# Kernel optimization log

Measured on AMD Instinct MI355X. Metric: run time of the kernel, lower is better.

The kernel has to match this reference:

```python
import jax, jax.numpy as jnp
import numpy as np

BETA = 0.25


def setup_inputs() -> dict:
    key = jax.random.key(0)
    k1, k2 = jax.random.split(key)
    B, D, H, W, K = 16, 256, 32, 32, 8192
    z_e = jax.random.normal(k1, (B, D, H, W), dtype=jnp.float32)
    # codebook init uniform(-1/K, 1/K) as in torch
    codebook = jax.random.uniform(k2, (K, D), dtype=jnp.float32,
                                  minval=-1.0 / K, maxval=1.0 / K)
    return {"z_e": z_e, "codebook": codebook}


def reference(z_e, codebook):
    B, D, H, W = z_e.shape
    K = codebook.shape[0]
    # (B, D, H, W) -> (BHW, D)
    z_flat = jnp.transpose(z_e, (0, 2, 3, 1)).reshape(-1, D)

    # distances computed under no_grad in torch -> stop_gradient here
    zf = jax.lax.stop_gradient(z_flat)
    cb = jax.lax.stop_gradient(codebook)
    # ||z||^2 + ||e||^2 - 2 z.e  -> (BHW, K)
    dist = ((zf * zf).sum(axis=1, keepdims=True)
            + (cb * cb).sum(axis=1)[None, :]
            - 2.0 * (zf @ cb.T))
    indices = jnp.argmin(dist, axis=1)  # (BHW,)

    # embedding gather, reshape back to (B, D, H, W)
    z_q_flat = codebook[indices]
    z_q = jnp.transpose(z_q_flat.reshape(B, H, W, D), (0, 3, 1, 2))

    # straight-through estimator
    z_q_st = z_e + jax.lax.stop_gradient(z_q - z_e)

    codebook_loss = jnp.mean((jax.lax.stop_gradient(z_q) - z_e) ** 2)
    commitment_loss = jnp.mean((z_q - jax.lax.stop_gradient(z_e)) ** 2)
    vq_loss = codebook_loss + BETA * commitment_loss

    # perplexity: one_hot(indices).mean(0) == counts / N
    N = z_flat.shape[0]
    counts = jnp.zeros((K,), dtype=z_flat.dtype).at[indices].add(1.0)
    avg_probs = counts / N
    perplexity = jnp.exp(-jnp.sum(avg_probs * jnp.log(avg_probs + 1e-10)))

    return (z_q_st, vq_loss, indices.reshape(B, H, W), perplexity)
```

## Files before the change

kernel.cpp:

```cpp
#include <hip/hip_runtime.h>

#define DD 256
#define KK 8192
#define HW 1024
#define NROWS 16384
#define NELEM 4194304
#define MT 32
#define MARGIN 6e-4f
#define WCAP 512
#define NT 256

typedef __attribute__((ext_vector_type(8))) short short8;
typedef __attribute__((ext_vector_type(4))) float f32x4;
typedef unsigned short ushort;
typedef unsigned int uint;
typedef unsigned long long u64;

__device__ __forceinline__ float np_pw128_sq(const float* p) {
  float r[8];
#pragma unroll
  for (int j = 0; j < 8; ++j) r[j] = __fmul_rn(p[j], p[j]);
  for (int i = 8; i < 128; i += 8) {
#pragma unroll
    for (int j = 0; j < 8; ++j)
      r[j] = __fadd_rn(r[j], __fmul_rn(p[i + j], p[i + j]));
  }
  return __fadd_rn(__fadd_rn(__fadd_rn(r[0], r[1]), __fadd_rn(r[2], r[3])),
                   __fadd_rn(__fadd_rn(r[4], r[5]), __fadd_rn(r[6], r[7])));
}

__device__ __forceinline__ ushort f2bf(float x) {
  uint u = __float_as_uint(x);
  u += 0x7FFF + ((u >> 16) & 1);
  return (ushort)(u >> 16);
}

__device__ __forceinline__ void emit8(ushort* __restrict__ zB, int g, int n16,
                                      int d0, const float* vv) {
  int s = d0 >> 5, q = (d0 >> 3) & 3;
  uint4 pk;
  pk.x = f2bf(vv[0]) | ((uint)f2bf(vv[1]) << 16);
  pk.y = f2bf(vv[2]) | ((uint)f2bf(vv[3]) << 16);
  pk.z = f2bf(vv[4]) | ((uint)f2bf(vv[5]) << 16);
  pk.w = f2bf(vv[6]) | ((uint)f2bf(vv[7]) << 16);
  *(uint4*)(zB + ((size_t)g * 512 + s * 64 + q * 16 + n16) * 8) = pk;
}

struct Top2 { float m1, m2; int i1; };

__device__ __forceinline__ void top2_upd(Top2& s, const f32x4 a,
                                         const f32x4 Bs, int ibase) {
  float d0 = fmaf(-2.f, a[0], Bs[0]);
  float d1 = fmaf(-2.f, a[1], Bs[1]);
  float d2 = fmaf(-2.f, a[2], Bs[2]);
  float d3 = fmaf(-2.f, a[3], Bs[3]);
  float lo01 = fminf(d0, d1), hi01 = fmaxf(d0, d1);
  int io01 = d1 < d0 ? ibase + 1 : ibase;
  float lo23 = fminf(d2, d3), hi23 = fmaxf(d2, d3);
  int io23 = d3 < d2 ? ibase + 3 : ibase + 2;
  float n1 = fminf(lo01, lo23);
  int ni = lo23 < lo01 ? io23 : io01;
  float n2 = fminf(fmaxf(lo01, lo23), fminf(hi01, hi23));
  s.m2 = fminf(fmaxf(s.m1, n1), fminf(s.m2, n2));
  s.i1 = n1 < s.m1 ? ni : s.i1;
  s.m1 = fminf(s.m1, n1);
}

__device__ __forceinline__ void top2_bfly(Top2& s, int off) {
  float om1 = __shfl_xor(s.m1, off);
  int oi1 = __shfl_xor(s.i1, off);
  float om2 = __shfl_xor(s.m2, off);
  s.m2 = fminf(fmaxf(s.m1, om1), fminf(s.m2, om2));
  s.i1 = om1 < s.m1 ? oi1 : s.i1;
  s.m1 = fminf(s.m1, om1);
}

__device__ __forceinline__ uint pack_m2(float m2, int i1) {
  uint u = __float_as_uint(m2);
  uint hi = u & 0xFFFF0000u;
  if ((u & 0x80000000u) && (u & 0xFFFFu)) hi += 0x10000u;
  return hi | (uint)i1;
}

__global__ __launch_bounds__(256) void vq_prep(const float* __restrict__ z,
                                               const float* __restrict__ cb,
                                               float* __restrict__ Bk,
                                               float* __restrict__ Arow,
                                               ushort* __restrict__ cbB,
                                               ushort* __restrict__ zB) {
  const int b = blockIdx.x, t = threadIdx.x;
  if (b < 32) {
    int k = b * 256 + t;
    const float* p = cb + (size_t)k * DD;
    Bk[k] = __fadd_rn(np_pw128_sq(p), np_pw128_sq(p + 128));
  } else if (b < 160) {
    int tid = (b - 32) * 256 + t;
    int n = tid >> 1, half = tid & 1;
    int bimg = n >> 10, hw = n & 1023;
    const float* zp = z + (size_t)bimg * DD * HW + hw;
    const int g = n >> 4, n16 = n & 15;
    const int dbase = half * 128;
    float r[8], vv[8];
#pragma unroll
    for (int j = 0; j < 8; ++j) {
      vv[j] = zp[(size_t)(dbase + j) * HW];
      r[j] = __fmul_rn(vv[j], vv[j]);
    }
    emit8(zB, g, n16, dbase, vv);
    for (int i = 8; i < 128; i += 8) {
      const int dd = dbase + i;
#pragma unroll
      for (int j = 0; j < 8; ++j) {
        vv[j] = zp[(size_t)(dd + j) * HW];
        r[j] = __fadd_rn(r[j], __fmul_rn(vv[j], vv[j]));
      }
      emit8(zB, g, n16, dd, vv);
    }
    float h = __fadd_rn(__fadd_rn(__fadd_rn(r[0], r[1]), __fadd_rn(r[2], r[3])),
                        __fadd_rn(__fadd_rn(r[4], r[5]), __fadd_rn(r[6], r[7])));
    float ho = __shfl_xor(h, 1);
    if (half == 0) Arow[n] = __fadd_rn(h, ho);
  } else {
    int tid = (b - 160) * 256 + t;
    int g = tid >> 9, s = (tid >> 6) & 7, lane = tid & 63;
    int code = g * 16 + (lane & 15);
    int dbase = s * 32 + (lane >> 4) * 8;
    const float* p = cb + (size_t)code * DD + dbase;
    ushort bb[8];
#pragma unroll
    for (int j = 0; j < 8; ++j) bb[j] = f2bf(p[j]);
    uint4 pk;
    pk.x = bb[0] | ((uint)bb[1] << 16);
    pk.y = bb[2] | ((uint)bb[3] << 16);
    pk.z = bb[4] | ((uint)bb[5] << 16);
    pk.w = bb[6] | ((uint)bb[7] << 16);
    *(uint4*)(cbB + (size_t)tid * 8) = pk;
  }
}

__global__ __launch_bounds__(256) void vq_screen(
    const ushort* __restrict__ zB, const ushort* __restrict__ cbB,
    const float* __restrict__ Bk, float* __restrict__ tA,
    uint* __restrict__ tB) {
  const int bid = blockIdx.x;
  const int rt = bid >> 1, cs = bid & 1;
  const int t = threadIdx.x;
  const int n0 = rt * MT;
  const int w = t >> 6, lane = t & 63;
  const int quad = lane >> 4, n16 = lane & 15;

  short8 aF[2][8];
#pragma unroll
  for (int rg = 0; rg < 2; ++rg) {
    const ushort* zp = zB + (size_t)(rt * 2 + rg) * 4096 + lane * 8;
#pragma unroll
    for (int s = 0; s < 8; ++s) aF[rg][s] = *(const short8*)(zp + s * 512);
  }

  const int gg0 = cs * 256 + w * 64;
  Top2 c0 = {3.4e38f, 3.4e38f, 0}, c1 = {3.4e38f, 3.4e38f, 0};

  short8 b0[8], b1[8];
  {
    const ushort* bp = cbB + (size_t)gg0 * 4096 + lane * 8;
#pragma unroll
    for (int s = 0; s < 8; ++s) b0[s] = *(const short8*)(bp + s * 512);
  }

  for (int gp = 0; gp < 32; ++gp) {
    const int gg = gg0 + gp * 2;
    {
      const ushort* bp = cbB + (size_t)(gg + 1) * 4096 + lane * 8;
#pragma unroll
      for (int s = 0; s < 8; ++s) b1[s] = *(const short8*)(bp + s * 512);
    }
    {
      f32x4 a0 = {0.f, 0.f, 0.f, 0.f}, a1 = {0.f, 0.f, 0.f, 0.f};
#pragma unroll
      for (int s = 0; s < 8; ++s) {
        a0 = __builtin_amdgcn_mfma_f32_16x16x32_bf16(b0[s], aF[0][s], a0, 0, 0, 0);
        a1 = __builtin_amdgcn_mfma_f32_16x16x32_bf16(b0[s], aF[1][s], a1, 0, 0, 0);
      }
      const f32x4 Bs = *(const f32x4*)(Bk + gg * 16 + quad * 4);
      top2_upd(c0, a0, Bs, quad * 4);
      top2_upd(c1, a1, Bs, quad * 4);
    }
    if (gp < 31) {
      const ushort* bp = cbB + (size_t)(gg + 2) * 4096 + lane * 8;
#pragma unroll
      for (int s = 0; s < 8; ++s) b0[s] = *(const short8*)(bp + s * 512);
    }
    {
      f32x4 a0 = {0.f, 0.f, 0.f, 0.f}, a1 = {0.f, 0.f, 0.f, 0.f};
#pragma unroll
      for (int s = 0; s < 8; ++s) {
        a0 = __builtin_amdgcn_mfma_f32_16x16x32_bf16(b1[s], aF[0][s], a0, 0, 0, 0);
        a1 = __builtin_amdgcn_mfma_f32_16x16x32_bf16(b1[s], aF[1][s], a1, 0, 0, 0);
      }
      const f32x4 Bs = *(const f32x4*)(Bk + (gg + 1) * 16 + quad * 4);
      top2_upd(c0, a0, Bs, 16 + quad * 4);
      top2_upd(c1, a1, Bs, 16 + quad * 4);
    }
    top2_bfly(c0, 16); top2_bfly(c0, 32);
    top2_bfly(c1, 16); top2_bfly(c1, 32);
    const size_t tbase = (size_t)(gg >> 1) * NROWS + n0;
    if (quad == 0) {
      tA[tbase + n16] = c0.m1;
      tB[tbase + n16] = pack_m2(c0.m2, c0.i1);
    } else if (quad == 1) {
      tA[tbase + 16 + n16] = c1.m1;
      tB[tbase + 16 + n16] = pack_m2(c1.m2, c1.i1);
    }
    c0.m1 = 3.4e38f; c0.m2 = 3.4e38f; c0.i1 = 0;
    c1.m1 = 3.4e38f; c1.m2 = 3.4e38f; c1.i1 = 0;
  }
}

__global__ __launch_bounds__(256) void vq_rerank(
    const float* __restrict__ z, const float* __restrict__ cb,
    const float* __restrict__ Bk, const float* __restrict__ Arow,
    const float* __restrict__ tA, const uint* __restrict__ tB,
    float* __restrict__ out, int* __restrict__ hist,
    float* __restrict__ loss_acc, u64* __restrict__ rowBest) {
  __shared__ float zt[MT][DD + 1];
  __shared__ float thr[MT];
  __shared__ float ArS[MT];
  __shared__ float partial[4][MT];
  __shared__ int wl[WCAP];
  __shared__ int wcnt;
  __shared__ int kwin[MT];
  __shared__ float lred[4];

  const int t = threadIdx.x;
  const int n0 = blockIdx.x * MT;
  const int bimg = n0 >> 10, hw0 = n0 & 1023;
  const float* zb = z + (size_t)bimg * DD * HW + hw0;

  if (t == 0) wcnt = 0;
  if (t < MT) ArS[t] = Arow[n0 + t];
  for (int li = t; li < MT * DD; li += 256) {
    int d = li >> 5, r = li & 31;
    zt[r][d] = zb[d * HW + r];
  }

  const int w = t >> 6, lane = t & 63;
  const int r = t & 31, j = t >> 5;

  float mn = 3.4e38f;
#pragma unroll 4
  for (int k = 0; k < 32; ++k)
    mn = fminf(mn, tA[(size_t)(j * 32 + k) * NROWS + n0 + r]);
  mn = fminf(mn, __shfl_xor(mn, 32));
  if (lane < 32) partial[w][r] = mn;
  __syncthreads();
  if (t < MT)
    thr[t] = fminf(fminf(partial[0][t], partial[1][t]),
                   fminf(partial[2][t], partial[3][t])) + MARGIN;
  __syncthreads();

  auto exact_one = [&](int rr, int code) {
    const float* cp = cb + (size_t)code * DD;
    float dot = 0.f;
#pragma unroll
    for (int d0 = 0; d0 < DD; d0 += 4) {
      float4 v = *(const float4*)(cp + d0);
      dot = fmaf(zt[rr][d0 + 0], v.x, dot);
      dot = fmaf(zt[rr][d0 + 1], v.y, dot);
      dot = fmaf(zt[rr][d0 + 2], v.z, dot);
      dot = fmaf(zt[rr][d0 + 3], v.w, dot);
    }
    float bd = __fsub_rn(__fadd_rn(ArS[rr], Bk[code]), __fmul_rn(2.f, dot));
    atomicMin(&rowBest[n0 + rr],
              ((u64)__float_as_uint(bd) << 32) | (unsigned)code);
  };

  const float th = thr[r];
  for (int k = 0; k < 32; ++k) {
    const int tile = j * 32 + k;
    const float a = tA[(size_t)tile * NROWS + n0 + r];
    if (a <= th) {
      const uint pk = tB[(size_t)tile * NROWS + n0 + r];
      const float m2f = __uint_as_float(pk & 0xFFFF0000u);
      if (m2f <= th) {
        for (int c = 0; c < 32; ++c) {
          int pos = atomicAdd(&wcnt, 1);
          if (pos < WCAP) wl[pos] = (r << 16) | (tile * 32 + c);
          else exact_one(r, tile * 32 + c);
        }
      } else {
        int pos = atomicAdd(&wcnt, 1);
        if (pos < WCAP) wl[pos] = (r << 16) | (tile * 32 + (int)(pk & 31u));
        else exact_one(r, tile * 32 + (int)(pk & 31u));
      }
    }
  }
  __syncthreads();

  const int cnt = min(wcnt, WCAP);
  for (int e = t; e < cnt; e += 256) {
    const int ent = wl[e];
    exact_one(ent >> 16, ent & 0xFFFF);
  }
  __syncthreads();

  if (t < MT) {
    u64 key = atomicMin(&rowBest[n0 + t], 0xFFFFFFFFFFFFFFFFull);
    int bi = (int)(key & 0xFFFFFFFFull);
    kwin[t] = bi;
    atomicAdd(&hist[bi], 1);
    out[(size_t)NELEM + 1 + n0 + t] = (float)bi;
  }
  __syncthreads();

  float lsum = 0.f;
  for (int it = 0; it < MT * DD / 256; ++it) {
    int li = it * 256 + t;
    int d = li >> 5, rr = li & 31;
    float ze = zt[rr][d];
    float zq = cb[(size_t)kwin[rr] * DD + d];
    float diff = __fsub_rn(zq, ze);
    float st = __fadd_rn(ze, diff);
    out[(size_t)(bimg * DD + d) * HW + hw0 + rr] = st;
    lsum = fmaf(diff, diff, lsum);
  }
#pragma unroll
  for (int off = 32; off > 0; off >>= 1) lsum += __shfl_down(lsum, off);
  if (lane == 0) lred[w] = lsum;
  __syncthreads();
  if (t == 0)
    atomicAdd(loss_acc, ((lred[0] + lred[1]) + (lred[2] + lred[3])));
}

__global__ __launch_bounds__(256) void vq_final(const int* __restrict__ hist,
                                                const float* __restrict__ loss,
                                                float* __restrict__ out) {
  __shared__ float sred[256];
  int t = threadIdx.x;
  float s = 0.f;
  for (int k = t; k < KK; k += 256) {
    float p = (float)hist[k] * (1.f / 16384.f);
    s += p * logf(p + 1e-10f);
  }
  sred[t] = s;
  __syncthreads();
  for (int off = 128; off > 0; off >>= 1) {
    if (t < off) sred[t] += sred[t + off];
    __syncthreads();
  }
  if (t == 0) {
    float L = loss[0] / (float)NELEM;
    out[NELEM] = 1.25f * L;
    out[(size_t)NELEM + 1 + NROWS] = expf(-sred[0]);
  }
}

extern "C" void kernel_launch(void* const* d_in, const int* in_sizes, int n_in,
                              void* d_out, int out_size, void* d_ws, size_t ws_size,
                              hipStream_t stream) {
  const float* z = (const float*)d_in[0];
  const float* cb = (const float*)d_in[1];
  float* out = (float*)d_out;

  float* wsf = (float*)d_ws;
  int* hist = (int*)d_ws;
  float* loss = wsf + 8192;
  float* Bk = wsf + 8448;
  float* Arow = wsf + 16640;
  u64* rowBest = (u64*)(wsf + 33024);
  ushort* cbB = (ushort*)(wsf + 65792);
  ushort* zB = (ushort*)(wsf + 1114368);
  float* tA = wsf + 3211520;
  uint* tB = (uint*)(wsf + 7405824);

  hipMemsetAsync(d_ws, 0, 8448 * sizeof(float), stream);
  hipMemsetAsync(rowBest, 0xFF, NROWS * sizeof(u64), stream);
  vq_prep<<<1184, 256, 0, stream>>>(z, cb, Bk, Arow, cbB, zB);
  vq_screen<<<(NROWS / MT) * 2, 256, 0, stream>>>(zB, cbB, Bk, tA, tB);
  vq_rerank<<<NROWS / MT, 256, 0, stream>>>(z, cb, Bk, Arow, tA, tB, out,
                                            hist, loss, rowBest);
  vq_final<<<1, 256, 0, stream>>>(hist, loss, out);
}
```

Baseline: 242.6 us.

## Fuse z bf16 conversion into screen kernel and split codebook into four slices

```diff
diff --git a/kernel.cpp b/kernel.cpp
--- a/kernel.cpp
+++ b/kernel.cpp
@@ -9,6 +9,7 @@
 #define MARGIN 6e-4f
 #define WCAP 512
 #define NT 256
+#define NSLICE 4
 
 typedef __attribute__((ext_vector_type(8))) short short8;
 typedef __attribute__((ext_vector_type(4))) float f32x4;
@@ -33,17 +34,6 @@
   uint u = __float_as_uint(x);
   u += 0x7FFF + ((u >> 16) & 1);
   return (ushort)(u >> 16);
-}
-
-__device__ __forceinline__ void emit8(ushort* __restrict__ zB, int g, int n16,
-                                      int d0, const float* vv) {
-  int s = d0 >> 5, q = (d0 >> 3) & 3;
-  uint4 pk;
-  pk.x = f2bf(vv[0]) | ((uint)f2bf(vv[1]) << 16);
-  pk.y = f2bf(vv[2]) | ((uint)f2bf(vv[3]) << 16);
-  pk.z = f2bf(vv[4]) | ((uint)f2bf(vv[5]) << 16);
-  pk.w = f2bf(vv[6]) | ((uint)f2bf(vv[7]) << 16);
-  *(uint4*)(zB + ((size_t)g * 512 + s * 64 + q * 16 + n16) * 8) = pk;
 }
 
 struct Top2 { float m1, m2; int i1; };
@@ -82,46 +72,16 @@
   return hi | (uint)i1;
 }
 
-__global__ __launch_bounds__(256) void vq_prep(const float* __restrict__ z,
-                                               const float* __restrict__ cb,
+__global__ __launch_bounds__(256) void vq_prep(const float* __restrict__ cb,
                                                float* __restrict__ Bk,
-                                               float* __restrict__ Arow,
-                                               ushort* __restrict__ cbB,
-                                               ushort* __restrict__ zB) {
+                                               ushort* __restrict__ cbB) {
   const int b = blockIdx.x, t = threadIdx.x;
   if (b < 32) {
     int k = b * 256 + t;
     const float* p = cb + (size_t)k * DD;
     Bk[k] = __fadd_rn(np_pw128_sq(p), np_pw128_sq(p + 128));
-  } else if (b < 160) {
+  } else {
     int tid = (b - 32) * 256 + t;
-    int n = tid >> 1, half = tid & 1;
-    int bimg = n >> 10, hw = n & 1023;
-    const float* zp = z + (size_t)bimg * DD * HW + hw;
-    const int g = n >> 4, n16 = n & 15;
-    const int dbase = half * 128;
-    float r[8], vv[8];
-#pragma unroll
-    for (int j = 0; j < 8; ++j) {
-      vv[j] = zp[(size_t)(dbase + j) * HW];
-      r[j] = __fmul_rn(vv[j], vv[j]);
-    }
-    emit8(zB, g, n16, dbase, vv);
-    for (int i = 8; i < 128; i += 8) {
-      const int dd = dbase + i;
-#pragma unroll
-      for (int j = 0; j < 8; ++j) {
-        vv[j] = zp[(size_t)(dd + j) * HW];
-        r[j] = __fadd_rn(r[j], __fmul_rn(vv[j], vv[j]));
-      }
-      emit8(zB, g, n16, dd, vv);
-    }
-    float h = __fadd_rn(__fadd_rn(__fadd_rn(r[0], r[1]), __fadd_rn(r[2], r[3])),
-                        __fadd_rn(__fadd_rn(r[4], r[5]), __fadd_rn(r[6], r[7])));
-    float ho = __shfl_xor(h, 1);
-    if (half == 0) Arow[n] = __fadd_rn(h, ho);
-  } else {
-    int tid = (b - 160) * 256 + t;
     int g = tid >> 9, s = (tid >> 6) & 7, lane = tid & 63;
     int code = g * 16 + (lane & 15);
     int dbase = s * 32 + (lane >> 4) * 8;
@@ -139,25 +99,36 @@
 }
 
 __global__ __launch_bounds__(256) void vq_screen(
-    const ushort* __restrict__ zB, const ushort* __restrict__ cbB,
+    const float* __restrict__ z, const ushort* __restrict__ cbB,
     const float* __restrict__ Bk, float* __restrict__ tA,
     uint* __restrict__ tB) {
+  __shared__ ushort ztB[MT][264];
   const int bid = blockIdx.x;
-  const int rt = bid >> 1, cs = bid & 1;
+  const int rt = bid >> 2, cs = bid & 3;
   const int t = threadIdx.x;
   const int n0 = rt * MT;
+  const int bimg = n0 >> 10, hw0 = n0 & 1023;
+  const float* zb = z + (size_t)bimg * DD * HW + hw0;
+
+  for (int li = t; li < MT * 128; li += 256) {
+    int r = li & 31, dp = li >> 5;
+    float v0 = zb[(size_t)(2 * dp) * HW + r];
+    float v1 = zb[(size_t)(2 * dp + 1) * HW + r];
+    *(uint*)&ztB[r][2 * dp] = (uint)f2bf(v0) | ((uint)f2bf(v1) << 16);
+  }
+  __syncthreads();
+
   const int w = t >> 6, lane = t & 63;
   const int quad = lane >> 4, n16 = lane & 15;
 
   short8 aF[2][8];
 #pragma unroll
-  for (int rg = 0; rg < 2; ++rg) {
-    const ushort* zp = zB + (size_t)(rt * 2 + rg) * 4096 + lane * 8;
-#pragma unroll
-    for (int s = 0; s < 8; ++s) aF[rg][s] = *(const short8*)(zp + s * 512);
-  }
-
-  const int gg0 = cs * 256 + w * 64;
+  for (int rg = 0; rg < 2; ++rg)
+#pragma unroll
+    for (int s = 0; s < 8; ++s)
+      aF[rg][s] = *(const short8*)&ztB[rg * 16 + n16][s * 32 + quad * 8];
+
+  const int gg0 = cs * 128 + w * 32;
   Top2 c0 = {3.4e38f, 3.4e38f, 0}, c1 = {3.4e38f, 3.4e38f, 0};
 
   short8 b0[8], b1[8];
@@ -167,7 +138,7 @@
     for (int s = 0; s < 8; ++s) b0[s] = *(const short8*)(bp + s * 512);
   }
 
-  for (int gp = 0; gp < 32; ++gp) {
+  for (int gp = 0; gp < 16; ++gp) {
     const int gg = gg0 + gp * 2;
     {
       const ushort* bp = cbB + (size_t)(gg + 1) * 4096 + lane * 8;
@@ -185,7 +156,7 @@
       top2_upd(c0, a0, Bs, quad * 4);
       top2_upd(c1, a1, Bs, quad * 4);
     }
-    if (gp < 31) {
+    if (gp < 15) {
       const ushort* bp = cbB + (size_t)(gg + 2) * 4096 + lane * 8;
 #pragma unroll
       for (int s = 0; s < 8; ++s) b0[s] = *(const short8*)(bp + s * 512);
@@ -218,10 +189,10 @@
 
 __global__ __launch_bounds__(256) void vq_rerank(
     const float* __restrict__ z, const float* __restrict__ cb,
-    const float* __restrict__ Bk, const float* __restrict__ Arow,
-    const float* __restrict__ tA, const uint* __restrict__ tB,
-    float* __restrict__ out, int* __restrict__ hist,
-    float* __restrict__ loss_acc, u64* __restrict__ rowBest) {
+    const float* __restrict__ Bk, const float* __restrict__ tA,
+    const uint* __restrict__ tB, float* __restrict__ out,
+    int* __restrict__ hist, float* __restrict__ loss_acc,
+    u64* __restrict__ rowBest) {
   __shared__ float zt[MT][DD + 1];
   __shared__ float thr[MT];
   __shared__ float ArS[MT];
@@ -237,7 +208,6 @@
   const float* zb = z + (size_t)bimg * DD * HW + hw0;
 
   if (t == 0) wcnt = 0;
-  if (t < MT) ArS[t] = Arow[n0 + t];
   for (int li = t; li < MT * DD; li += 256) {
     int d = li >> 5, r = li & 31;
     zt[r][d] = zb[d * HW + r];
@@ -253,9 +223,15 @@
   mn = fminf(mn, __shfl_xor(mn, 32));
   if (lane < 32) partial[w][r] = mn;
   __syncthreads();
-  if (t < MT)
+  if (t < MT) {
     thr[t] = fminf(fminf(partial[0][t], partial[1][t]),
                    fminf(partial[2][t], partial[3][t])) + MARGIN;
+  } else if (t >= 128 && t < 192) {
+    int rr = (t - 128) >> 1, half = t & 1;
+    float h = np_pw128_sq(&zt[rr][half * 128]);
+    float ho = __shfl_xor(h, 1);
+    if (half == 0) ArS[rr] = __fadd_rn(h, ho);
+  }
   __syncthreads();
 
   auto exact_one = [&](int rr, int code) {
@@ -365,18 +341,16 @@
   int* hist = (int*)d_ws;
   float* loss = wsf + 8192;
   float* Bk = wsf + 8448;
-  float* Arow = wsf + 16640;
-  u64* rowBest = (u64*)(wsf + 33024);
-  ushort* cbB = (ushort*)(wsf + 65792);
-  ushort* zB = (ushort*)(wsf + 1114368);
-  float* tA = wsf + 3211520;
-  uint* tB = (uint*)(wsf + 7405824);
+  u64* rowBest = (u64*)(wsf + 16640);
+  ushort* cbB = (ushort*)(wsf + 49408);
+  float* tA = wsf + 1097984;
+  uint* tB = (uint*)(wsf + 5292288);
 
   hipMemsetAsync(d_ws, 0, 8448 * sizeof(float), stream);
   hipMemsetAsync(rowBest, 0xFF, NROWS * sizeof(u64), stream);
-  vq_prep<<<1184, 256, 0, stream>>>(z, cb, Bk, Arow, cbB, zB);
-  vq_screen<<<(NROWS / MT) * 2, 256, 0, stream>>>(zB, cbB, Bk, tA, tB);
-  vq_rerank<<<NROWS / MT, 256, 0, stream>>>(z, cb, Bk, Arow, tA, tB, out,
+  vq_prep<<<1056, 256, 0, stream>>>(cb, Bk, cbB);
+  vq_screen<<<(NROWS / MT) * NSLICE, 256, 0, stream>>>(z, cbB, Bk, tA, tB);
+  vq_rerank<<<NROWS / MT, 256, 0, stream>>>(z, cb, Bk, tA, tB, out,
                                             hist, loss, rowBest);
   vq_final<<<1, 256, 0, stream>>>(hist, loss, out);
 }
```

After: 238.4 us. About the same (-1.7%).
